# Optimization experiments

Measured on AMD Instinct MI355X. Metric: run time of the kernel, lower is better.

Reference implementation:

```python
import jax, jax.numpy as jnp
import numpy as np

N_CB, K, CD = 8, 1024, 64  # n_codebooks, codebook_size, codebook_dim
B, T = 8, 2048
D = N_CB * CD


def setup_inputs() -> dict:
    key = jax.random.key(0)
    k1, k2 = jax.random.split(key)
    z = jax.random.normal(k1, (B, T, D), dtype=jnp.float32)
    codebooks = jax.random.normal(k2, (N_CB, K, CD), dtype=jnp.float32)
    return {"z": z, "codebooks": codebooks}


def reference(z, codebooks):
    Bz, Tz, Dz = z.shape
    n_cb, k, cd = codebooks.shape
    z_chunks = z.reshape(Bz, Tz, n_cb, cd)

    res = z_chunks[:, :, 0, :]  # running residual [B,T,cd]
    q_chunks, idx_list, logits_list = [], [], []
    for i in range(n_cb):
        cb = codebooks[i]  # [K, cd]
        # squared euclidean distance: |r|^2 + |c|^2 - 2 r.c  -> [B,T,K]
        dist = ((res ** 2).sum(-1, keepdims=True)
                + (cb ** 2).sum(-1)
                - 2.0 * jnp.einsum('btd,kd->btk', res, cb))
        logits_list.append(-dist)
        idx = jnp.argmin(dist, axis=-1)  # [B,T]
        idx_list.append(idx)
        q = cb[idx]  # gather -> [B,T,cd]
        q_chunks.append(q)
        if i < n_cb - 1:
            # quantization error is added to the next chunk's residual
            res = z_chunks[:, :, i + 1, :] + (res - jax.lax.stop_gradient(q))

    z_q_diff = jnp.stack(q_chunks, axis=2).reshape(Bz, Tz, Dz)
    # straight-through: value == z_q_diff; grads flow to both z and z_q_diff
    z_q = z + jax.lax.stop_gradient(z_q_diff - z) + (z_q_diff - jax.lax.stop_gradient(z_q_diff))
    indices = jnp.stack(idx_list, axis=1)   # [B, n_cb, T]
    logits = jnp.stack(logits_list, axis=1)  # [B, n_cb, T, K]
    return z_q, indices, logits
```

## Files before the change

### kernel.cpp

```cpp
#include <hip/hip_runtime.h>

namespace {
constexpr int NCB = 8;
constexpr int K   = 1024;
constexpr int CD  = 64;
constexpr int T   = 2048;
constexpr int B   = 8;
constexpr int D   = NCB * CD;
constexpr int TM  = 32;
constexpr int KT  = 128;
constexpr int LDK = CD + 4;
constexpr int NTH = 256;

constexpr long ZQ_OFF  = 0;
constexpr long IDX_OFF = (long)B * T * D;
constexpr long LG_OFF  = IDX_OFF + (long)B * NCB * T;
}

__global__ __launch_bounds__(NTH, 2)
void rvq_kernel(const float* __restrict__ Z, const float* __restrict__ CB,
                float* __restrict__ out)
{
    __shared__ float sCb[KT * LDK];
    __shared__ float sRes[TM * LDK];
    __shared__ float sCn2[KT];
    __shared__ float sRn2[TM];
    __shared__ int   sBest[TM];

    const int tid = threadIdx.x;
    const int kth = tid & 31;
    const int grp = tid >> 5;
    const int gt0 = blockIdx.x * TM;
    const int b   = gt0 / T;
    const int t0  = gt0 % T;

    float* __restrict__ zq  = out + ZQ_OFF;
    float* __restrict__ ido = out + IDX_OFF;
    float* __restrict__ lgo = out + LG_OFF;

    #pragma unroll 1
    for (int s = 0; s < NCB; ++s) {
        __syncthreads();

        #pragma unroll
        for (int r = 0; r < (TM * CD) / (4 * NTH); ++r) {
            const int f4  = tid + r * NTH;
            const int tok = f4 >> 4;
            const int dv  = f4 & 15;
            const float4 zv = *(const float4*)(Z + (long)(gt0 + tok) * D + s * CD + dv * 4);
            float4* rp = (float4*)(&sRes[tok * LDK + dv * 4]);
            if (s == 0) {
                *rp = zv;
            } else {
                const int best = sBest[tok];
                const float4 qv = *(const float4*)(CB + (long)((s - 1) * K + best) * CD + dv * 4);
                float4 rv = *rp;
                rv.x = zv.x + (rv.x - qv.x);
                rv.y = zv.y + (rv.y - qv.y);
                rv.z = zv.z + (rv.z - qv.z);
                rv.w = zv.w + (rv.w - qv.w);
                *rp = rv;
                *(float4*)(zq + (long)(gt0 + tok) * D + (s - 1) * CD + dv * 4) = qv;
            }
        }
        __syncthreads();

        if (tid < TM) {
            const float4* rr = (const float4*)(&sRes[tid * LDK]);
            float a = 0.f;
            #pragma unroll
            for (int c = 0; c < CD / 4; ++c) {
                const float4 v = rr[c];
                a += v.x * v.x + v.y * v.y + v.z * v.z + v.w * v.w;
            }
            sRn2[tid] = a;
        }

        float bestv[4];
        int   besti[4];
        #pragma unroll
        for (int m = 0; m < 4; ++m) { bestv[m] = -3.4e38f; besti[m] = 0; }

        #pragma unroll 1
        for (int tile = 0; tile < K / KT; ++tile) {
            __syncthreads();

            const float4* src = (const float4*)(CB + (long)(s * K + tile * KT) * CD);
            #pragma unroll
            for (int r = 0; r < (KT * CD) / (4 * NTH); ++r) {
                const int f4 = tid + r * NTH;
                const int k  = f4 >> 4;
                const int dv = f4 & 15;
                *(float4*)(&sCb[k * LDK + dv * 4]) = src[f4];
            }
            __syncthreads();

            if (tid < KT) {
                const float4* cr = (const float4*)(&sCb[tid * LDK]);
                float a = 0.f;
                #pragma unroll
                for (int c = 0; c < CD / 4; ++c) {
                    const float4 v = cr[c];
                    a += v.x * v.x + v.y * v.y + v.z * v.z + v.w * v.w;
                }
                sCn2[tid] = a;
            }
            __syncthreads();

            float acc[4][4];
            #pragma unroll
            for (int m = 0; m < 4; ++m)
                #pragma unroll
                for (int j = 0; j < 4; ++j) acc[m][j] = 0.f;

            const float4* crow[4];
            #pragma unroll
            for (int j = 0; j < 4; ++j)
                crow[j] = (const float4*)(&sCb[(j * 32 + kth) * LDK]);
            const float4* rrow[4];
            #pragma unroll
            for (int m = 0; m < 4; ++m)
                rrow[m] = (const float4*)(&sRes[(grp * 4 + m) * LDK]);

            #pragma unroll
            for (int dc = 0; dc < CD / 4; ++dc) {
                float4 rv[4];
                #pragma unroll
                for (int m = 0; m < 4; ++m) rv[m] = rrow[m][dc];
                #pragma unroll
                for (int j = 0; j < 4; ++j) {
                    const float4 cv = crow[j][dc];
                    #pragma unroll
                    for (int m = 0; m < 4; ++m) {
                        acc[m][j] += rv[m].x * cv.x + rv[m].y * cv.y
                                   + rv[m].z * cv.z + rv[m].w * cv.w;
                    }
                }
            }

            const int kbase = tile * KT;
            float* lp0 = lgo + ((long)((b * NCB + s) * T + t0 + grp * 4) * K) + kbase + kth;
            #pragma unroll
            for (int m = 0; m < 4; ++m) {
                const float rn2 = sRn2[grp * 4 + m];
                float* lp = lp0 + (long)m * K;
                #pragma unroll
                for (int j = 0; j < 4; ++j) {
                    const float cn2 = sCn2[j * 32 + kth];
                    const float lg = 2.0f * acc[m][j] - (rn2 + cn2);
                    lp[j * 32] = lg;
                    const int kidx = kbase + j * 32 + kth;
                    if (lg > bestv[m]) { bestv[m] = lg; besti[m] = kidx; }
                }
            }
        }

        #pragma unroll
        for (int m = 0; m < 4; ++m) {
            float v  = bestv[m];
            int   ii = besti[m];
            #pragma unroll
            for (int off = 16; off > 0; off >>= 1) {
                const float ov = __shfl_xor(v, off);
                const int   oi = __shfl_xor(ii, off);
                if (ov > v || (ov == v && oi < ii)) { v = ov; ii = oi; }
            }
            if (kth == 0) {
                sBest[grp * 4 + m] = ii;
                ido[(long)(b * NCB + s) * T + t0 + grp * 4 + m] = (float)ii;
            }
        }
    }

    __syncthreads();
    #pragma unroll
    for (int r = 0; r < (TM * CD) / (4 * NTH); ++r) {
        const int f4  = tid + r * NTH;
        const int tok = f4 >> 4;
        const int dv  = f4 & 15;
        const int best = sBest[tok];
        const float4 qv = *(const float4*)(CB + (long)(7 * K + best) * CD + dv * 4);
        *(float4*)(zq + (long)(gt0 + tok) * D + 7 * CD + dv * 4) = qv;
    }
}

extern "C" void kernel_launch(void* const* d_in, const int* in_sizes, int n_in,
                              void* d_out, int out_size, void* d_ws, size_t ws_size,
                              hipStream_t stream)
{
    const float* Z   = (const float*)d_in[0];
    const float* CBp = (const float*)d_in[1];
    float* out = (float*)d_out;

    dim3 grid((B * T) / TM);
    dim3 block(NTH);
    hipLaunchKernelGGL(rvq_kernel, grid, block, 0, stream, Z, CBp, out);
}
```

Before: 907.3 us.

## Use split-bf16 MFMA for distances with top-3 candidates and exact fp32 rescoring

Adds a prep kernel that splits each codebook into hi/lo bf16 MFMA fragments and precomputes codebook norms into workspace. The main kernel computes residual-codebook dot products with bf16x3-style MFMA instead of scalar FP32 FMAs from shared memory, and writes logits with nontemporal stores. Each lane keeps its top-3 candidates per token, and the block rescores the merged candidates in exact FP32 to pick the argmin. The path depends on a workspace being provided, otherwise it falls back to the old kernel. The split-bf16 logits carry a small precision loss.

```diff
diff --git a/kernel.cpp b/kernel.cpp
--- a/kernel.cpp
+++ b/kernel.cpp
@@ -1,4 +1,7 @@
 #include <hip/hip_runtime.h>
+
+typedef float f32x4 __attribute__((ext_vector_type(4)));
+typedef short s16x8 __attribute__((ext_vector_type(8)));
 
 namespace {
 constexpr int NCB = 8;
@@ -8,35 +11,94 @@
 constexpr int B   = 8;
 constexpr int D   = NCB * CD;
 constexpr int TM  = 32;
-constexpr int KT  = 128;
+constexpr int NTH = 256;
 constexpr int LDK = CD + 4;
-constexpr int NTH = 256;
 
 constexpr long ZQ_OFF  = 0;
 constexpr long IDX_OFF = (long)B * T * D;
 constexpr long LG_OFF  = IDX_OFF + (long)B * NCB * T;
+
+constexpr size_t FRAG_SH8   = (size_t)NCB * 64 * 2 * 2 * 64;
+constexpr size_t FRAG_BYTES = FRAG_SH8 * 16;
+constexpr size_t CN2_OFF    = FRAG_BYTES;
+constexpr size_t WS_NEEDED  = FRAG_BYTES + (size_t)NCB * K * sizeof(float);
+}
+
+__device__ __forceinline__ unsigned short f2bf(float x) {
+    unsigned u = __float_as_uint(x);
+    unsigned r = u + 0x7fffu + ((u >> 16) & 1u);
+    return (unsigned short)(r >> 16);
+}
+__device__ __forceinline__ float bf2f(unsigned short h) {
+    return __uint_as_float(((unsigned)h) << 16);
+}
+
+#define MFMA16(a, b, c) __builtin_amdgcn_mfma_f32_16x16x32_bf16((a), (b), (c), 0, 0, 0)
+
+__global__ __launch_bounds__(NTH)
+void rvq_prep(const float* __restrict__ CB, char* __restrict__ ws)
+{
+    const int tid = threadIdx.x;
+    if (blockIdx.x < 256) {
+        const int f    = blockIdx.x * NTH + tid;
+        const int lane = f & 63;
+        const int ks   = (f >> 6) & 1;
+        const int cfg  = (f >> 7) & 63;
+        const int s    = f >> 13;
+        const int cw   = cfg * 16 + (lane & 15);
+        const int d0   = ks * 32 + (lane >> 4) * 8;
+        const float* src = CB + ((size_t)(s * K + cw)) * CD + d0;
+        const float4 x0 = *(const float4*)src;
+        const float4 x1 = *(const float4*)(src + 4);
+        float xs[8] = {x0.x, x0.y, x0.z, x0.w, x1.x, x1.y, x1.z, x1.w};
+        s16x8 hv, lv;
+        #pragma unroll
+        for (int e = 0; e < 8; ++e) {
+            const unsigned short hb = f2bf(xs[e]);
+            hv[e] = (short)hb;
+            lv[e] = (short)f2bf(xs[e] - bf2f(hb));
+        }
+        s16x8* dst = (s16x8*)ws + ((((size_t)(s * 64 + cfg) * 2 + ks) * 2 + 0) * 64 + lane);
+        dst[0]  = hv;
+        dst[64] = lv;
+    } else {
+        const int t = (blockIdx.x - 256) * NTH + tid;
+        const float4* src = (const float4*)(CB + (size_t)t * CD);
+        float a = 0.f;
+        #pragma unroll
+        for (int c = 0; c < CD / 4; ++c) {
+            const float4 v = src[c];
+            a += v.x * v.x + v.y * v.y + v.z * v.z + v.w * v.w;
+        }
+        ((float*)(ws + CN2_OFF))[t] = a;
+    }
 }
 
 __global__ __launch_bounds__(NTH, 2)
-void rvq_kernel(const float* __restrict__ Z, const float* __restrict__ CB,
-                float* __restrict__ out)
+void rvq_mfma(const float* __restrict__ Z, const float* __restrict__ CB,
+              float* __restrict__ out, const char* __restrict__ ws)
 {
-    __shared__ float sCb[KT * LDK];
     __shared__ float sRes[TM * LDK];
-    __shared__ float sCn2[KT];
     __shared__ float sRn2[TM];
     __shared__ int   sBest[TM];
-
-    const int tid = threadIdx.x;
-    const int kth = tid & 31;
-    const int grp = tid >> 5;
-    const int gt0 = blockIdx.x * TM;
-    const int b   = gt0 / T;
-    const int t0  = gt0 % T;
+    __shared__ float sPV[TM][12];
+    __shared__ int   sPI[TM][12];
+
+    const int tid  = threadIdx.x;
+    const int lane = tid & 63;
+    const int wid  = tid >> 6;
+    const int l15  = lane & 15;
+    const int lg4  = lane >> 4;
+    const int gt0  = blockIdx.x * TM;
+    const int b    = gt0 / T;
+    const int t0   = gt0 % T;
+    const int c0   = wid * 256;
 
     float* __restrict__ zq  = out + ZQ_OFF;
     float* __restrict__ ido = out + IDX_OFF;
     float* __restrict__ lgo = out + LG_OFF;
+    const s16x8* __restrict__ fragAll = (const s16x8*)ws;
+    const float* __restrict__ cn2g    = (const float*)(ws + CN2_OFF);
 
     #pragma unroll 1
     for (int s = 0; s < NCB; ++s) {
@@ -76,98 +138,168 @@
             sRn2[tid] = a;
         }
 
-        float bestv[4];
-        int   besti[4];
-        #pragma unroll
-        for (int m = 0; m < 4; ++m) { bestv[m] = -3.4e38f; besti[m] = 0; }
-
-        #pragma unroll 1
-        for (int tile = 0; tile < K / KT; ++tile) {
-            __syncthreads();
-
-            const float4* src = (const float4*)(CB + (long)(s * K + tile * KT) * CD);
-            #pragma unroll
-            for (int r = 0; r < (KT * CD) / (4 * NTH); ++r) {
-                const int f4 = tid + r * NTH;
-                const int k  = f4 >> 4;
-                const int dv = f4 & 15;
-                *(float4*)(&sCb[k * LDK + dv * 4]) = src[f4];
-            }
-            __syncthreads();
-
-            if (tid < KT) {
-                const float4* cr = (const float4*)(&sCb[tid * LDK]);
-                float a = 0.f;
-                #pragma unroll
-                for (int c = 0; c < CD / 4; ++c) {
-                    const float4 v = cr[c];
-                    a += v.x * v.x + v.y * v.y + v.z * v.z + v.w * v.w;
-                }
-                sCn2[tid] = a;
-            }
-            __syncthreads();
-
-            float acc[4][4];
-            #pragma unroll
-            for (int m = 0; m < 4; ++m)
-                #pragma unroll
-                for (int j = 0; j < 4; ++j) acc[m][j] = 0.f;
-
-            const float4* crow[4];
-            #pragma unroll
-            for (int j = 0; j < 4; ++j)
-                crow[j] = (const float4*)(&sCb[(j * 32 + kth) * LDK]);
-            const float4* rrow[4];
-            #pragma unroll
-            for (int m = 0; m < 4; ++m)
-                rrow[m] = (const float4*)(&sRes[(grp * 4 + m) * LDK]);
-
-            #pragma unroll
-            for (int dc = 0; dc < CD / 4; ++dc) {
-                float4 rv[4];
-                #pragma unroll
-                for (int m = 0; m < 4; ++m) rv[m] = rrow[m][dc];
-                #pragma unroll
-                for (int j = 0; j < 4; ++j) {
-                    const float4 cv = crow[j][dc];
+        s16x8 Ahi[2][2], Alo[2][2];
+        #pragma unroll
+        for (int rf = 0; rf < 2; ++rf) {
+            #pragma unroll
+            for (int ks = 0; ks < 2; ++ks) {
+                const float* rp = &sRes[(rf * 16 + l15) * LDK + ks * 32 + lg4 * 8];
+                const float4 x0 = *(const float4*)rp;
+                const float4 x1 = *(const float4*)(rp + 4);
+                float xs[8] = {x0.x, x0.y, x0.z, x0.w, x1.x, x1.y, x1.z, x1.w};
+                s16x8 h, l;
+                #pragma unroll
+                for (int e = 0; e < 8; ++e) {
+                    const unsigned short hb = f2bf(xs[e]);
+                    h[e] = (short)hb;
+                    l[e] = (short)f2bf(xs[e] - bf2f(hb));
+                }
+                Ahi[rf][ks] = h;
+                Alo[rf][ks] = l;
+            }
+        }
+        __syncthreads();
+
+        float rn2v[2][4];
+        #pragma unroll
+        for (int rf = 0; rf < 2; ++rf)
+            #pragma unroll
+            for (int r = 0; r < 4; ++r)
+                rn2v[rf][r] = sRn2[rf * 16 + lg4 * 4 + r];
+
+        float cn2v[16];
+        #pragma unroll
+        for (int cf = 0; cf < 16; ++cf)
+            cn2v[cf] = cn2g[s * K + c0 + cf * 16 + l15];
+
+        float* pr0 = lgo + ((long)((b * NCB + s) * T) + t0 + lg4 * 4) * K + c0 + l15;
+        float* pr1 = pr0 + (long)16 * K;
+
+        const int kb = c0 + l15;
+        float tv[2][4][3];
+        int   ti[2][4][3];
+        #pragma unroll
+        for (int rf = 0; rf < 2; ++rf)
+            #pragma unroll
+            for (int r = 0; r < 4; ++r)
+                #pragma unroll
+                for (int p = 0; p < 3; ++p) { tv[rf][r][p] = -3.4e38f; ti[rf][r][p] = 0x7fffffff; }
+
+        const s16x8* fb = fragAll + (size_t)s * 16384 + (size_t)wid * 16 * 256 + lane;
+        s16x8 bb[3][4];
+        #pragma unroll
+        for (int j = 0; j < 4; ++j) bb[0][j] = fb[0 * 256 + j * 64];
+        #pragma unroll
+        for (int j = 0; j < 4; ++j) bb[1][j] = fb[1 * 256 + j * 64];
+
+        #pragma unroll
+        for (int cf = 0; cf < 16; ++cf) {
+            if (cf + 2 < 16) {
+                #pragma unroll
+                for (int j = 0; j < 4; ++j)
+                    bb[(cf + 2) % 3][j] = fb[(size_t)(cf + 2) * 256 + j * 64];
+            }
+            const s16x8 b0 = bb[cf % 3][0];
+            const s16x8 b1 = bb[cf % 3][1];
+            const s16x8 b2 = bb[cf % 3][2];
+            const s16x8 b3 = bb[cf % 3][3];
+
+            f32x4 a0 = {0.f, 0.f, 0.f, 0.f};
+            f32x4 a1 = {0.f, 0.f, 0.f, 0.f};
+            a0 = MFMA16(Alo[0][0], b1, a0);  a1 = MFMA16(Alo[1][0], b1, a1);
+            a0 = MFMA16(Ahi[0][0], b1, a0);  a1 = MFMA16(Ahi[1][0], b1, a1);
+            a0 = MFMA16(Alo[0][0], b0, a0);  a1 = MFMA16(Alo[1][0], b0, a1);
+            a0 = MFMA16(Ahi[0][0], b0, a0);  a1 = MFMA16(Ahi[1][0], b0, a1);
+            a0 = MFMA16(Alo[0][1], b3, a0);  a1 = MFMA16(Alo[1][1], b3, a1);
+            a0 = MFMA16(Ahi[0][1], b3, a0);  a1 = MFMA16(Ahi[1][1], b3, a1);
+            a0 = MFMA16(Alo[0][1], b2, a0);  a1 = MFMA16(Alo[1][1], b2, a1);
+            a0 = MFMA16(Ahi[0][1], b2, a0);  a1 = MFMA16(Ahi[1][1], b2, a1);
+
+            const int ki = kb + cf * 16;
+            #pragma unroll
+            for (int rf = 0; rf < 2; ++rf) {
+                const f32x4 av = rf ? a1 : a0;
+                float* prb = rf ? pr1 : pr0;
+                #pragma unroll
+                for (int r = 0; r < 4; ++r) {
+                    const float lg = 2.0f * av[r] - (rn2v[rf][r] + cn2v[cf]);
+                    __builtin_nontemporal_store(lg, prb + (long)r * K + cf * 16);
+                    if (lg > tv[rf][r][2]) {
+                        if (lg > tv[rf][r][1]) {
+                            if (lg > tv[rf][r][0]) {
+                                tv[rf][r][2] = tv[rf][r][1]; ti[rf][r][2] = ti[rf][r][1];
+                                tv[rf][r][1] = tv[rf][r][0]; ti[rf][r][1] = ti[rf][r][0];
+                                tv[rf][r][0] = lg;           ti[rf][r][0] = ki;
+                            } else {
+                                tv[rf][r][2] = tv[rf][r][1]; ti[rf][r][2] = ti[rf][r][1];
+                                tv[rf][r][1] = lg;           ti[rf][r][1] = ki;
+                            }
+                        } else {
+                            tv[rf][r][2] = lg; ti[rf][r][2] = ki;
+                        }
+                    }
+                }
+            }
+        }
+
+        #pragma unroll
+        for (int rf = 0; rf < 2; ++rf) {
+            #pragma unroll
+            for (int r = 0; r < 4; ++r) {
+                float c0v = tv[rf][r][0], c1v = tv[rf][r][1], c2v = tv[rf][r][2];
+                int   c0i = ti[rf][r][0], c1i = ti[rf][r][1], c2i = ti[rf][r][2];
+                const int tok = rf * 16 + lg4 * 4 + r;
+                #pragma unroll
+                for (int p = 0; p < 3; ++p) {
+                    float rv_ = c0v; int ri_ = c0i;
                     #pragma unroll
-                    for (int m = 0; m < 4; ++m) {
-                        acc[m][j] += rv[m].x * cv.x + rv[m].y * cv.y
-                                   + rv[m].z * cv.z + rv[m].w * cv.w;
+                    for (int off = 8; off > 0; off >>= 1) {
+                        const float ov = __shfl_xor(rv_, off);
+                        const int   oi = __shfl_xor(ri_, off);
+                        if (ov > rv_ || (ov == rv_ && oi < ri_)) { rv_ = ov; ri_ = oi; }
                     }
-                }
-            }
-
-            const int kbase = tile * KT;
-            float* lp0 = lgo + ((long)((b * NCB + s) * T + t0 + grp * 4) * K) + kbase + kth;
-            #pragma unroll
-            for (int m = 0; m < 4; ++m) {
-                const float rn2 = sRn2[grp * 4 + m];
-                float* lp = lp0 + (long)m * K;
-                #pragma unroll
-                for (int j = 0; j < 4; ++j) {
-                    const float cn2 = sCn2[j * 32 + kth];
-                    const float lg = 2.0f * acc[m][j] - (rn2 + cn2);
-                    lp[j * 32] = lg;
-                    const int kidx = kbase + j * 32 + kth;
-                    if (lg > bestv[m]) { bestv[m] = lg; besti[m] = kidx; }
-                }
-            }
-        }
-
-        #pragma unroll
-        for (int m = 0; m < 4; ++m) {
-            float v  = bestv[m];
-            int   ii = besti[m];
-            #pragma unroll
-            for (int off = 16; off > 0; off >>= 1) {
-                const float ov = __shfl_xor(v, off);
-                const int   oi = __shfl_xor(ii, off);
-                if (ov > v || (ov == v && oi < ii)) { v = ov; ii = oi; }
-            }
-            if (kth == 0) {
-                sBest[grp * 4 + m] = ii;
-                ido[(long)(b * NCB + s) * T + t0 + grp * 4 + m] = (float)ii;
+                    if (l15 == 0) { sPV[tok][wid * 3 + p] = rv_; sPI[tok][wid * 3 + p] = ri_; }
+                    const bool mine = (c0i == ri_);
+                    c0v = mine ? c1v : c0v;  c0i = mine ? c1i : c0i;
+                    c1v = mine ? c2v : c1v;  c1i = mine ? c2i : c1i;
+                    c2v = mine ? -3.4e38f : c2v;
+                }
+            }
+        }
+        __syncthreads();
+
+        {
+            const int tok = tid >> 3;
+            const int j   = tid & 7;
+            const float rn2 = sRn2[tok];
+            const float4* rr = (const float4*)(&sRes[tok * LDK]);
+            float bv = -3.4e38f; int bi = 0x7fffffff;
+            #pragma unroll
+            for (int pass = 0; pass < 2; ++pass) {
+                const int n = j + pass * 8;
+                if (n < 12) {
+                    const int ci = sPI[tok][n];
+                    const float4* cc = (const float4*)(CB + (long)(s * K + ci) * CD);
+                    float acc = 0.f;
+                    #pragma unroll
+                    for (int dc = 0; dc < CD / 4; ++dc) {
+                        const float4 rv = rr[dc];
+                        const float4 cv = cc[dc];
+                        acc += rv.x * cv.x + rv.y * cv.y + rv.z * cv.z + rv.w * cv.w;
+                    }
+                    const float lg = 2.0f * acc - (rn2 + cn2g[s * K + ci]);
+                    if (lg > bv || (lg == bv && ci < bi)) { bv = lg; bi = ci; }
+                }
+            }
+            #pragma unroll
+            for (int off = 4; off > 0; off >>= 1) {
+                const float ov = __shfl_xor(bv, off);
+                const int   oi = __shfl_xor(bi, off);
+                if (ov > bv || (ov == bv && oi < bi)) { bv = ov; bi = oi; }
+            }
+            if (j == 0) {
+                sBest[tok] = bi;
+                ido[(long)(b * NCB + s) * T + t0 + tok] = (float)bi;
             }
         }
     }
@@ -184,6 +316,175 @@
     }
 }
 
+namespace {
+constexpr int KT = 128;
+}
+
+__global__ __launch_bounds__(NTH, 2)
+void rvq_kernel_fallback(const float* __restrict__ Z, const float* __restrict__ CB,
+                         float* __restrict__ out)
+{
+    __shared__ float sCb[KT * LDK];
+    __shared__ float sRes[TM * LDK];
+    __shared__ float sCn2[KT];
+    __shared__ float sRn2[TM];
+    __shared__ int   sBest[TM];
+
+    const int tid = threadIdx.x;
+    const int kth = tid & 31;
+    const int grp = tid >> 5;
+    const int gt0 = blockIdx.x * TM;
+    const int b   = gt0 / T;
+    const int t0  = gt0 % T;
+
+    float* __restrict__ zq  = out + ZQ_OFF;
+    float* __restrict__ ido = out + IDX_OFF;
+    float* __restrict__ lgo = out + LG_OFF;
+
+    #pragma unroll 1
+    for (int s = 0; s < NCB; ++s) {
+        __syncthreads();
+        #pragma unroll
+        for (int r = 0; r < (TM * CD) / (4 * NTH); ++r) {
+            const int f4  = tid + r * NTH;
+            const int tok = f4 >> 4;
+            const int dv  = f4 & 15;
+            const float4 zv = *(const float4*)(Z + (long)(gt0 + tok) * D + s * CD + dv * 4);
+            float4* rp = (float4*)(&sRes[tok * LDK + dv * 4]);
+            if (s == 0) {
+                *rp = zv;
+            } else {
+                const int best = sBest[tok];
+                const float4 qv = *(const float4*)(CB + (long)((s - 1) * K + best) * CD + dv * 4);
+                float4 rv = *rp;
+                rv.x = zv.x + (rv.x - qv.x);
+                rv.y = zv.y + (rv.y - qv.y);
+                rv.z = zv.z + (rv.z - qv.z);
+                rv.w = zv.w + (rv.w - qv.w);
+                *rp = rv;
+                *(float4*)(zq + (long)(gt0 + tok) * D + (s - 1) * CD + dv * 4) = qv;
+            }
+        }
+        __syncthreads();
+
+        if (tid < TM) {
+            const float4* rr = (const float4*)(&sRes[tid * LDK]);
+            float a = 0.f;
+            #pragma unroll
+            for (int c = 0; c < CD / 4; ++c) {
+                const float4 v = rr[c];
+                a += v.x * v.x + v.y * v.y + v.z * v.z + v.w * v.w;
+            }
+            sRn2[tid] = a;
+        }
+
+        float bestv[4];
+        int   besti[4];
+        #pragma unroll
+        for (int m = 0; m < 4; ++m) { bestv[m] = -3.4e38f; besti[m] = 0; }
+
+        #pragma unroll 1
+        for (int tile = 0; tile < K / KT; ++tile) {
+            __syncthreads();
+            const float4* src = (const float4*)(CB + (long)(s * K + tile * KT) * CD);
+            #pragma unroll
+            for (int r = 0; r < (KT * CD) / (4 * NTH); ++r) {
+                const int f4 = tid + r * NTH;
+                const int k  = f4 >> 4;
+                const int dv = f4 & 15;
+                *(float4*)(&sCb[k * LDK + dv * 4]) = src[f4];
+            }
+            __syncthreads();
+
+            if (tid < KT) {
+                const float4* cr = (const float4*)(&sCb[tid * LDK]);
+                float a = 0.f;
+                #pragma unroll
+                for (int c = 0; c < CD / 4; ++c) {
+                    const float4 v = cr[c];
+                    a += v.x * v.x + v.y * v.y + v.z * v.z + v.w * v.w;
+                }
+                sCn2[tid] = a;
+            }
+            __syncthreads();
+
+            float acc[4][4];
+            #pragma unroll
+            for (int m = 0; m < 4; ++m)
+                #pragma unroll
+                for (int j = 0; j < 4; ++j) acc[m][j] = 0.f;
+
+            const float4* crow[4];
+            #pragma unroll
+            for (int j = 0; j < 4; ++j)
+                crow[j] = (const float4*)(&sCb[(j * 32 + kth) * LDK]);
+            const float4* rrow[4];
+            #pragma unroll
+            for (int m = 0; m < 4; ++m)
+                rrow[m] = (const float4*)(&sRes[(grp * 4 + m) * LDK]);
+
+            #pragma unroll
+            for (int dc = 0; dc < CD / 4; ++dc) {
+                float4 rv[4];
+                #pragma unroll
+                for (int m = 0; m < 4; ++m) rv[m] = rrow[m][dc];
+                #pragma unroll
+                for (int j = 0; j < 4; ++j) {
+                    const float4 cv = crow[j][dc];
+                    #pragma unroll
+                    for (int m = 0; m < 4; ++m) {
+                        acc[m][j] += rv[m].x * cv.x + rv[m].y * cv.y
+                                   + rv[m].z * cv.z + rv[m].w * cv.w;
+                    }
+                }
+            }
+
+            const int kbase = tile * KT;
+            float* lp0 = lgo + ((long)((b * NCB + s) * T + t0 + grp * 4) * K) + kbase + kth;
+            #pragma unroll
+            for (int m = 0; m < 4; ++m) {
+                const float rn2 = sRn2[grp * 4 + m];
+                float* lp = lp0 + (long)m * K;
+                #pragma unroll
+                for (int j = 0; j < 4; ++j) {
+                    const float cn2 = sCn2[j * 32 + kth];
+                    const float lg = 2.0f * acc[m][j] - (rn2 + cn2);
+                    lp[j * 32] = lg;
+                    const int kidx = kbase + j * 32 + kth;
+                    if (lg > bestv[m]) { bestv[m] = lg; besti[m] = kidx; }
+                }
+            }
+        }
+
+        #pragma unroll
+        for (int m = 0; m < 4; ++m) {
+            float v  = bestv[m];
+            int   ii = besti[m];
+            #pragma unroll
+            for (int off = 16; off > 0; off >>= 1) {
+                const float ov = __shfl_xor(v, off);
+                const int   oi = __shfl_xor(ii, off);
+                if (ov > v || (ov == v && oi < ii)) { v = ov; ii = oi; }
+            }
+            if (kth == 0) {
+                sBest[grp * 4 + m] = ii;
+                ido[(long)(b * NCB + s) * T + t0 + grp * 4 + m] = (float)ii;
+            }
+        }
+    }
+
+    __syncthreads();
+    #pragma unroll
+    for (int r = 0; r < (TM * CD) / (4 * NTH); ++r) {
+        const int f4  = tid + r * NTH;
+        const int tok = f4 >> 4;
+        const int dv  = f4 & 15;
+        const int best = sBest[tok];
+        const float4 qv = *(const float4*)(CB + (long)(7 * K + best) * CD + dv * 4);
+        *(float4*)(zq + (long)(gt0 + tok) * D + 7 * CD + dv * 4) = qv;
+    }
+}
+
 extern "C" void kernel_launch(void* const* d_in, const int* in_sizes, int n_in,
                               void* d_out, int out_size, void* d_ws, size_t ws_size,
                               hipStream_t stream)
@@ -192,7 +493,12 @@
     const float* CBp = (const float*)d_in[1];
     float* out = (float*)d_out;
 
-    dim3 grid((B * T) / TM);
-    dim3 block(NTH);
-    hipLaunchKernelGGL(rvq_kernel, grid, block, 0, stream, Z, CBp, out);
-}
+    if (d_ws != nullptr && ws_size >= WS_NEEDED) {
+        hipLaunchKernelGGL(rvq_prep, dim3(288), dim3(NTH), 0, stream, CBp, (char*)d_ws);
+        hipLaunchKernelGGL(rvq_mfma, dim3((B * T) / TM), dim3(NTH), 0, stream,
+                           Z, CBp, out, (const char*)d_ws);
+    } else {
+        hipLaunchKernelGGL(rvq_kernel_fallback, dim3((B * T) / TM), dim3(NTH), 0, stream,
+                           Z, CBp, out);
+    }
+}
```

New measurement: 738.7 us. 18.6% less time.
